# Kernel tuning notes

Hardware: AMD Instinct MI355X
Metric: run time of the kernel (lower is better)

Reference implementation:

```python
import jax, jax.numpy as jnp
import numpy as np
import math

C = 256          # embed_dims
NH = 8           # num_heads
FFN = 512        # int(embed_dims * ffn_ratio)
SPLITS = ((1, 1, 1), (2, 2, 2), (4, 4, 4), (8, 8, 8))
S = len(SPLITS)
B, Z, Hd, W = 1, 16, 16, 16


def setup_inputs() -> dict:
    key = jax.random.key(0)
    ks = jax.random.split(key, 10)
    n = lambda k, sh: jax.random.normal(k, sh, dtype=jnp.float32) * 0.02
    return {
        "x": jax.random.normal(ks[0], (B, C, Z, Hd, W), dtype=jnp.float32),
        "intra_wqkv": n(ks[1], (S, 3 * C, C)), "intra_bqkv": jnp.zeros((S, 3 * C), jnp.float32),
        "intra_wout": n(ks[2], (S, C, C)), "intra_bout": jnp.zeros((S, C), jnp.float32),
        "intra_ln_g": jnp.ones((S, C), jnp.float32), "intra_ln_b": jnp.zeros((S, C), jnp.float32),
        "inter_wqkv": n(ks[3], (S, 3 * C, C)), "inter_bqkv": jnp.zeros((S, 3 * C), jnp.float32),
        "inter_wout": n(ks[4], (S, C, C)), "inter_bout": jnp.zeros((S, C), jnp.float32),
        "inter_ln_g": jnp.ones((S, C), jnp.float32), "inter_ln_b": jnp.zeros((S, C), jnp.float32),
        "ffn_w1": n(ks[5], (S, FFN, C)), "ffn_b1": jnp.zeros((S, FFN), jnp.float32),
        "ffn_w2": n(ks[6], (S, C, FFN)), "ffn_b2": jnp.zeros((S, C), jnp.float32),
        "fuse_w": n(ks[7], (C, S * C)),
        "bn_g": jnp.ones((C,), jnp.float32), "bn_b": jnp.zeros((C,), jnp.float32),
    }


def _ln(x, g, b, eps=1e-5):
    m = x.mean(-1, keepdims=True)
    v = jnp.var(x, axis=-1, keepdims=True)
    return (x - m) / jnp.sqrt(v + eps) * g + b


def _mha(x, wqkv, bqkv, wout, bout):
    # x: [Bn, L, C]; torch nn.MultiheadAttention math (dropout=0)
    Bn, L, Cc = x.shape
    D = Cc // NH
    qkv = x @ wqkv.T + bqkv
    q, k, v = jnp.split(qkv, 3, axis=-1)
    q = q.reshape(Bn, L, NH, D)
    k = k.reshape(Bn, L, NH, D)
    v = v.reshape(Bn, L, NH, D)
    att = jax.nn.softmax(jnp.einsum('blhd,bmhd->bhlm', q, k) / math.sqrt(D), axis=-1)
    o = jnp.einsum('bhlm,bmhd->blhd', att, v).reshape(Bn, L, Cc)
    return o @ wout.T + bout


def reference(x, intra_wqkv, intra_bqkv, intra_wout, intra_bout, intra_ln_g, intra_ln_b,
              inter_wqkv, inter_bqkv, inter_wout, inter_bout, inter_ln_g, inter_ln_b,
              ffn_w1, ffn_b1, ffn_w2, ffn_b2, fuse_w, bn_g, bn_b):
    b, c, z, h, w = x.shape
    outs = []
    for i, (sx, sy, sz) in enumerate(SPLITS):
        bx, by, bz = w // sx, h // sy, z // sz  # dims divisible -> no padding path
        nb, bs = sx * sy * sz, bx * by * bz
        # carve blocks: [b,c,z,h,w] -> [b*nb, bs, c]
        xp = jnp.transpose(x, (0, 2, 3, 4, 1))
        t = xp.reshape(b, sz, bz, sy, by, sx, bx, c)
        t = jnp.transpose(t, (0, 1, 3, 5, 2, 4, 6, 7)).reshape(b * nb, bs, c)
        # intra-block self-attention + residual + LN
        t = _ln(t + _mha(t, intra_wqkv[i], intra_bqkv[i], intra_wout[i], intra_bout[i]),
                intra_ln_g[i], intra_ln_b[i])
        # inter-block attention on block means
        r = t.reshape(b, nb, bs, c).mean(2)  # [b, nb, c]
        r = _ln(r + _mha(r, inter_wqkv[i], inter_bqkv[i], inter_wout[i], inter_bout[i]),
                inter_ln_g[i], inter_ln_b[i])
        t = t.reshape(b, nb, bs, c) + r[:, :, None, :]
        # FFN (exact GELU) with residual
        hid = jax.nn.gelu(t @ ffn_w1[i].T + ffn_b1[i], approximate=False)
        t = t + (hid @ ffn_w2[i].T + ffn_b2[i])
        # un-carve back to [b,c,z,h,w]
        xo = t.reshape(b, sz, sy, sx, bz, by, bx, c)
        xo = jnp.transpose(xo, (0, 1, 4, 2, 5, 3, 6, 7)).reshape(b, z, h, w, c)
        xo = jnp.transpose(xo, (0, 4, 1, 2, 3))
        outs.append(xo + x)
    fused = jnp.concatenate(outs, axis=1)  # [b, 4c, z, h, w]
    y = jnp.einsum('bkzhw,ck->bczhw', fused, fuse_w)  # 1x1x1 Conv3d, no bias
    # BatchNorm3d in training mode: biased batch stats
    m = y.mean(axis=(0, 2, 3, 4))
    v = jnp.var(y, axis=(0, 2, 3, 4))
    bc = lambda a: a[None, :, None, None, None]
    y = (y - bc(m)) / jnp.sqrt(bc(v) + 1e-5) * bc(bn_g) + bc(bn_b)
    return jax.nn.relu(y)
```

## Files before the change

### kernel.cpp

```cpp
#include <hip/hip_runtime.h>
#include <math.h>

typedef __attribute__((ext_vector_type(8))) short s16x8;
typedef __attribute__((ext_vector_type(4))) short s16x4;
typedef __attribute__((ext_vector_type(4))) float f32x4;

__device__ __forceinline__ float b2f(unsigned short u) {
    union { unsigned u; float f; } x;
    x.u = ((unsigned)u) << 16;
    return x.f;
}
__device__ __forceinline__ unsigned short f2b(float f) {
    union { float f; unsigned u; } x;
    x.f = f;
    unsigned u = x.u;
    return (unsigned short)((u + 0x7FFFu + ((u >> 16) & 1u)) >> 16);
}
__device__ __forceinline__ f32x4 mfma16(s16x8 a, s16x8 b, f32x4 c) {
    return __builtin_amdgcn_mfma_f32_16x16x32_bf16(a, b, c, 0, 0, 0);
}
__device__ __forceinline__ float gelu_exact(float x) {
    return 0.5f * x * (1.0f + erff(x * 0.70710678118654752440f));
}
__device__ __forceinline__ void gload_lds16(const void* g, void* l) {
    __builtin_amdgcn_global_load_lds(
        (const __attribute__((address_space(1))) unsigned int*)g,
        (__attribute__((address_space(3))) unsigned int*)l, 16, 0, 0);
}
__device__ __forceinline__ int voxof(int blk, int pos, int logs, int lbsz) {
    int bm = (1 << lbsz) - 1, sm = (1 << logs) - 1;
    int ix = pos & bm, iy = (pos >> lbsz) & bm, iz = pos >> (2 * lbsz);
    int gx = blk & sm, gy = (blk >> logs) & sm, gz = blk >> (2 * logs);
    return (((gz << lbsz) + iz) << 8) + (((gy << lbsz) + iy) << 4) + ((gx << lbsz) + ix);
}
__device__ __forceinline__ int blkof(int v, int logs, int lbsz) {
    int gx = (v & 15) >> lbsz, gy = ((v >> 4) & 15) >> lbsz, gz = ((v >> 8) & 15) >> lbsz;
    return (((gz << logs) + gy) << logs) + gx;
}

__global__ __launch_bounds__(256) void prologue_k(
    const float* w0, const float* w1, const float* w2, const float* w3,
    const float* w4, const float* w5, const float* w6,
    unsigned short* __restrict__ wdst, const float* __restrict__ x,
    float* __restrict__ Xt, unsigned short* __restrict__ Xtb,
    float* __restrict__ Rb) {
    __shared__ float tile[32][33];
    int bx = blockIdx.x;
    if (bx < 3328) {
        int i = (bx * 256 + threadIdx.x) * 4;
        const float* s; int off;
        if (i < 786432)        { s = w0; off = 0; }
        else if (i < 1048576)  { s = w1; off = 786432; }
        else if (i < 1835008)  { s = w2; off = 1048576; }
        else if (i < 2097152)  { s = w3; off = 1835008; }
        else if (i < 2621440)  { s = w4; off = 2097152; }
        else if (i < 3145728)  { s = w5; off = 2621440; }
        else                   { s = w6; off = 3145728; }
        float4 v = *reinterpret_cast<const float4*>(s + (i - off));
        wdst[i + 0] = f2b(v.x); wdst[i + 1] = f2b(v.y);
        wdst[i + 2] = f2b(v.z); wdst[i + 3] = f2b(v.w);
    } else if (bx < 4352) {
        int t = bx - 3328;
        int v0 = (t & 127) * 32, c0 = (t >> 7) * 32;
        int tx = threadIdx.x & 31, ty = threadIdx.x >> 5;
#pragma unroll
        for (int j = 0; j < 32; j += 8)
            tile[ty + j][tx] = x[(size_t)(c0 + ty + j) * 4096 + v0 + tx];
        __syncthreads();
#pragma unroll
        for (int j = 0; j < 32; j += 8) {
            float v = tile[tx][ty + j];
            size_t o = (size_t)(v0 + ty + j) * 256 + c0 + tx;
            Xt[o] = v;
            Xtb[o] = f2b(v);
        }
    } else {
        int idx = ((bx - 4352) * 256 + threadIdx.x) * 4;
        if (idx < 149760) {
            float4 z4 = make_float4(0.f, 0.f, 0.f, 0.f);
            *reinterpret_cast<float4*>(Rb + idx) = z4;
        }
    }
}

template <int MFR, int HASB, int ACT, int OBF, int VT, int AF32, int EPI, int ZS>
__global__ __launch_bounds__(256) void gemm_k(
    const void* __restrict__ Aptr, const unsigned short* __restrict__ W,
    const float* __restrict__ bias, void* __restrict__ outp,
    int M, int N, int K, int ldC,
    long zsA, long zsW, long zsB, long zsC,
    unsigned short* __restrict__ vt, int mtot, long zsV,
    const void* __restrict__ Tresv, const float* __restrict__ RLNres,
    const float* __restrict__ Xres) {
    constexpr int BM = 32 * MFR;
    __shared__ unsigned short As[BM * 64];
    __shared__ unsigned short Ws[64 * 64];
    const int z = blockIdx.z;
    const int logs = (ZS == 1) ? z : 0;
    const int lbsz = (ZS == 1) ? (4 - z) : 4;
    const int goffc[4] = {0, 1, 9, 73};
    const int Mzc[4] = {1, 8, 64, 512};
    const int Me = (ZS == 2) ? Mzc[z] : M;
    const int m0 = blockIdx.y * BM, n0 = blockIdx.x * 64;
    if (ZS == 2 && m0 >= Me) return;
    const unsigned short* Ab = (const unsigned short*)Aptr +
        ((AF32 == 0 || AF32 == 3) ? ((size_t)z * zsA + (ZS == 2 ? (size_t)goffc[z] * K : 0)) : 0);
    const float* Af = (const float*)Aptr +
        ((AF32 == 1 || AF32 == 2) ? ((size_t)z * zsA + (ZS == 2 ? (size_t)goffc[z] * K : 0)) : 0);
    W += (size_t)z * zsW;
    const float* biasz = bias + (HASB ? (size_t)z * zsB : 0);
    char* outc = (char*)outp +
        ((size_t)z * zsC + (ZS == 2 ? (size_t)goffc[z] * ldC : 0)) * ((OBF || EPI) ? 2 : 4);
    const float* RLNz = RLNres + (ZS == 1 ? goffc[z] * 256 : 0);
    const unsigned short* Tzb = (const unsigned short*)Tresv + (ZS == 1 ? (size_t)z * 1048576 : 0);

    const int tid = threadIdx.x;
    const int wave = tid >> 6, lane = tid & 63;
    const int l15 = lane & 15, l4 = lane >> 4;
    const int wr = wave >> 1, wc = wave & 1;
    const int srow = lane >> 3;
    const int schunk = (lane & 7) ^ srow;
    f32x4 acc[MFR][2] = {};
    for (int k0 = 0; k0 < K; k0 += 64) {
        s16x8 sreg[MFR];
        if (AF32) {
#pragma unroll
            for (int i = 0; i < MFR; ++i) {
                int ca = wave * MFR + i;
                int gr = m0 + ca * 8 + srow;
                gr = gr < Me ? gr : (Me - 1);
                s16x8 pk;
                if (AF32 == 3) {
                    s16x8 tb = *reinterpret_cast<const s16x8*>(Ab + (size_t)gr * K + k0 + schunk * 8);
                    const float* rl = RLNz + (size_t)blkof(gr, logs, lbsz) * 256 + k0 + schunk * 8;
#pragma unroll
                    for (int e = 0; e < 8; ++e) pk[e] = (short)f2b(b2f((unsigned short)tb[e]) + rl[e]);
                } else {
                    const float* src = Af + (size_t)gr * K + k0 + schunk * 8;
                    float4 u = *reinterpret_cast<const float4*>(src);
                    float4 w2 = *reinterpret_cast<const float4*>(src + 4);
                    if (AF32 == 2) {
                        const float* rl = RLNz + (size_t)blkof(gr, logs, lbsz) * 256 + k0 + schunk * 8;
                        float4 a = *reinterpret_cast<const float4*>(rl);
                        float4 b = *reinterpret_cast<const float4*>(rl + 4);
                        u.x += a.x; u.y += a.y; u.z += a.z; u.w += a.w;
                        w2.x += b.x; w2.y += b.y; w2.z += b.z; w2.w += b.w;
                    }
                    pk[0] = (short)f2b(u.x); pk[1] = (short)f2b(u.y);
                    pk[2] = (short)f2b(u.z); pk[3] = (short)f2b(u.w);
                    pk[4] = (short)f2b(w2.x); pk[5] = (short)f2b(w2.y);
                    pk[6] = (short)f2b(w2.z); pk[7] = (short)f2b(w2.w);
                }
                sreg[i] = pk;
            }
        }
        __syncthreads();
        if (AF32) {
#pragma unroll
            for (int i = 0; i < MFR; ++i) {
                int ca = wave * MFR + i;
                *reinterpret_cast<s16x8*>((char*)As + ca * 1024 + lane * 16) = sreg[i];
            }
        } else {
#pragma unroll
            for (int i = 0; i < MFR; ++i) {
                int ca = wave * MFR + i;
                int gr = m0 + ca * 8 + srow;
                gr = gr < Me ? gr : (Me - 1);
                gload_lds16(Ab + (size_t)gr * K + k0 + schunk * 8, (char*)As + ca * 1024);
            }
        }
#pragma unroll
        for (int i = 0; i < 2; ++i) {
            int cb = wave * 2 + i;
            int gr = n0 + cb * 8 + srow;
            gload_lds16(W + (size_t)gr * K + k0 + schunk * 8, (char*)Ws + cb * 1024);
        }
        asm volatile("s_waitcnt vmcnt(0)" ::: "memory");
        __syncthreads();
#pragma unroll
        for (int ks = 0; ks < 2; ++ks) {
            s16x8 af[MFR], bf[2];
#pragma unroll
            for (int mf = 0; mf < MFR; ++mf) {
                int row = wr * (MFR * 16) + mf * 16 + l15;
                int ch = (ks * 4 + l4) ^ (row & 7);
                af[mf] = *reinterpret_cast<const s16x8*>((char*)As + row * 128 + ch * 16);
            }
#pragma unroll
            for (int nf = 0; nf < 2; ++nf) {
                int row = wc * 32 + nf * 16 + l15;
                int ch = (ks * 4 + l4) ^ (row & 7);
                bf[nf] = *reinterpret_cast<const s16x8*>((char*)Ws + row * 128 + ch * 16);
            }
#pragma unroll
            for (int mf = 0; mf < MFR; ++mf)
#pragma unroll
                for (int nf = 0; nf < 2; ++nf)
                    acc[mf][nf] = mfma16(af[mf], bf[nf], acc[mf][nf]);
        }
    }
#pragma unroll
    for (int nf = 0; nf < 2; ++nf) {
        int n = n0 + wc * 32 + nf * 16 + l15;
        float bv = HASB ? biasz[n] : 0.0f;
#pragma unroll
        for (int mf = 0; mf < MFR; ++mf) {
            float vr[4];
#pragma unroll
            for (int r = 0; r < 4; ++r) {
                int m = m0 + wr * (MFR * 16) + mf * 16 + l4 * 4 + r;
                float v = acc[mf][nf][r] + bv;
                if (ACT == 1) v = gelu_exact(v);
                vr[r] = v;
                if (m < Me) {
                    size_t co = (size_t)m * ldC + n;
                    if (EPI == 1) {
                        v += b2f(Tzb[(size_t)m * 256 + n]) +
                             RLNz[(size_t)blkof(m, logs, lbsz) * 256 + n] +
                             Xres[(size_t)m * 256 + n];
                        ((unsigned short*)outc)[co] = f2b(v);
                    } else if (OBF) {
                        ((unsigned short*)outc)[co] = f2b(v);
                    } else {
                        ((float*)outc)[co] = v;
                    }
                }
            }
            if (VT) {
                if ((ZS != 2 || z == 3) && n >= 512) {
                    s16x4 pk;
#pragma unroll
                    for (int r = 0; r < 4; ++r) pk[r] = (short)f2b(vr[r]);
                    int mb = m0 + wr * (MFR * 16) + mf * 16 + l4 * 4;
                    *reinterpret_cast<s16x4*>(vt + (size_t)z * zsV + (size_t)(n - 512) * mtot + mb) = pk;
                }
            }
        }
    }
}

__global__ __launch_bounds__(256) void attn_mfma2_k(
    const unsigned short* __restrict__ QKV, const unsigned short* __restrict__ Vtg,
    unsigned short* __restrict__ Opart, float* __restrict__ ML,
    int L, int Mtok, float cscale, int logs, int lbsz) {
    const int blk = blockIdx.z >> 3, h = blockIdx.z & 7;
    const int KS = gridDim.y, ks = blockIdx.y;
    const int wave = threadIdx.x >> 6, lane = threadIdx.x & 63;
    const int l15 = lane & 15, l4 = lane >> 4;
    const int q0 = blockIdx.x * 64 + wave * 16;

    __shared__ unsigned short Kl[2048];
    __shared__ unsigned short Vl[2048];
    __shared__ unsigned short Pl[4096];
    char* Plw = (char*)Pl + wave * 2048;

    const int qvox = voxof(blk, q0 + l15, logs, lbsz);
    s16x8 qf = *reinterpret_cast<const s16x8*>(QKV + (size_t)qvox * 768 + h * 32 + l4 * 8);

    f32x4 o0 = {}, o1 = {};
    float lR = 0.f;

    const int krow = threadIdx.x >> 2, kch = threadIdx.x & 3;
    const int kcol = (kch ^ (krow & 3)) * 8;
    const int vd = threadIdx.x >> 3, vc = threadIdx.x & 7;
    const int vrun = (vc ^ (vd & 7)) * 8;

    const int nt = L / (64 * KS);
    const int kb0 = ks * (L / KS);
    const int vstep = voxof(blk, kb0 + 64, logs, lbsz) - voxof(blk, kb0, logs, lbsz);
    const unsigned short* ksrc =
        QKV + (size_t)voxof(blk, kb0 + krow, logs, lbsz) * 768 + 256 + h * 32 + kcol;
    const unsigned short* vsrc =
        Vtg + (size_t)(h * 32 + vd) * Mtok + voxof(blk, kb0 + vrun, logs, lbsz);
    const size_t kadv = (size_t)vstep * 768;
    char* kdst = (char*)Kl + wave * 1024;
    char* vdst = (char*)Vl + wave * 1024;

    for (int it = 0; it < nt; ++it) {
        __syncthreads();
        gload_lds16(ksrc, kdst);
        gload_lds16(vsrc, vdst);
        ksrc += kadv; vsrc += vstep;
        asm volatile("s_waitcnt vmcnt(0)" ::: "memory");
        __syncthreads();

        f32x4 st[4];
        const f32x4 zz = {0.f, 0.f, 0.f, 0.f};
#pragma unroll
        for (int t4 = 0; t4 < 4; ++t4) {
            s16x8 kf = *reinterpret_cast<const s16x8*>(
                (char*)Kl + (t4 * 16 + l15) * 64 + ((l4 ^ (l15 & 3)) << 4));
            st[t4] = mfma16(kf, qf, zz);
        }
        float rsum = 0.f;
#pragma unroll
        for (int t4 = 0; t4 < 4; ++t4) {
            float p0 = exp2f(st[t4][0] * cscale);
            float p1 = exp2f(st[t4][1] * cscale);
            float p2 = exp2f(st[t4][2] * cscale);
            float p3 = exp2f(st[t4][3] * cscale);
            rsum += (p0 + p1) + (p2 + p3);
            unsigned d0, d1;
            asm("v_cvt_pk_bf16_f32 %0, %1, %2" : "=v"(d0) : "v"(p0), "v"(p1));
            asm("v_cvt_pk_bf16_f32 %0, %1, %2" : "=v"(d1) : "v"(p2), "v"(p3));
            int kcw = t4 * 2 + (l4 >> 1);
            uint2 w; w.x = d0; w.y = d1;
            *reinterpret_cast<uint2*>(Plw + l15 * 128 + ((kcw ^ (l15 & 7)) * 16) + (l4 & 1) * 8) = w;
        }
        rsum += __shfl_xor(rsum, 16);
        rsum += __shfl_xor(rsum, 32);
        lR += rsum;
#pragma unroll
        for (int kstep = 0; kstep < 2; ++kstep) {
            int kcr = kstep * 4 + l4;
            s16x8 pf = *reinterpret_cast<const s16x8*>(Plw + l15 * 128 + ((kcr ^ (l15 & 7)) * 16));
            s16x8 vf0 = *reinterpret_cast<const s16x8*>((char*)Vl + l15 * 128 + ((kcr ^ (l15 & 7)) * 16));
            s16x8 vf1 = *reinterpret_cast<const s16x8*>((char*)Vl + (16 + l15) * 128 + ((kcr ^ (l15 & 7)) * 16));
            o0 = mfma16(pf, vf0, o0);
            o1 = mfma16(pf, vf1, o1);
        }
    }
    float li[4];
#pragma unroll
    for (int r = 0; r < 4; ++r) li[r] = 1.0f / __shfl(lR, l4 * 4 + r);
#pragma unroll
    for (int r = 0; r < 4; ++r) {
        size_t row = ((size_t)ks * Mtok + voxof(blk, q0 + l4 * 4 + r, logs, lbsz)) * 256 + h * 32;
        Opart[row + l15] = f2b(o0[r] * li[r]);
        Opart[row + 16 + l15] = f2b(o1[r] * li[r]);
    }
    if (l4 == 0) ML[((size_t)ks * Mtok + qvox) * 8 + h] = lR;
}

__global__ __launch_bounds__(256) void attn_combine_k(
    const unsigned short* __restrict__ Opart, const float* __restrict__ ML,
    unsigned short* __restrict__ O, int TotTok, int KS,
    long zOp, long zML, long zO) {
    int z = blockIdx.y, row = blockIdx.x, c = threadIdx.x, h = c >> 5;
    Opart += (size_t)z * zOp;
    ML += (size_t)z * zML;
    O += (size_t)z * zO;
    float osum = 0.f, lsum = 0.f;
    for (int ks = 0; ks < KS; ++ks) {
        float l = ML[((size_t)ks * TotTok + row) * 8 + h];
        lsum += l;
        osum += l * b2f(Opart[((size_t)ks * TotTok + row) * 256 + c]);
    }
    O[(size_t)row * 256 + c] = f2b(osum / lsum);
}

__global__ __launch_bounds__(256) void attn_f32i_k(const unsigned short* __restrict__ QKVA2,
                                                   unsigned short* __restrict__ ObfA,
                                                   float scale) {
    int y = blockIdx.y;
    int z, blk, h, L, logs, lbsz;
    if (y < 512) { z = 2; blk = y >> 3; h = y & 7; L = 64; logs = 2; lbsz = 2; }
    else {
        z = 3; int yy = y - 512; blk = yy >> 3; h = yy & 7; L = 8; logs = 3; lbsz = 1;
        if (blockIdx.x != 0) return;
    }
    const unsigned short* QKV = QKVA2 + (size_t)(z - 2) * 3145728;
    unsigned short* O = ObfA + (size_t)z * 1048576;
    const int tid = threadIdx.x, r = tid >> 3, li = tid & 7;
    const int qr = blockIdx.x * 32 + r;
    const int qrc = (qr < L) ? qr : 0;
    const int qvox = voxof(blk, qrc, logs, lbsz);

    float q[32];
    {
        const unsigned short* qp = QKV + (size_t)qvox * 768 + h * 32;
#pragma unroll
        for (int d8 = 0; d8 < 4; ++d8) {
            s16x8 v = *reinterpret_cast<const s16x8*>(qp + d8 * 8);
#pragma unroll
            for (int e = 0; e < 8; ++e) q[d8 * 8 + e] = b2f((unsigned short)v[e]) * scale;
        }
    }
    float l = 0.f;
    float o[32];
#pragma unroll
    for (int d = 0; d < 32; ++d) o[d] = 0.f;

    __shared__ float Kl[32][36];
    __shared__ float Vl[32][36];
    const int krow = tid >> 3, kd = (tid & 7) * 4;
    const int nt = (L + 31) / 32;
    for (int kt = 0; kt < nt; ++kt) {
        int key = kt * 32 + krow;
        float4 kv = make_float4(0.f, 0.f, 0.f, 0.f);
        float4 vv = make_float4(0.f, 0.f, 0.f, 0.f);
        if (key < L) {
            int kvox = voxof(blk, key, logs, lbsz);
            s16x4 k4 = *reinterpret_cast<const s16x4*>(QKV + (size_t)kvox * 768 + 256 + h * 32 + kd);
            s16x4 v4 = *reinterpret_cast<const s16x4*>(QKV + (size_t)kvox * 768 + 512 + h * 32 + kd);
            kv = make_float4(b2f((unsigned short)k4[0]), b2f((unsigned short)k4[1]),
                             b2f((unsigned short)k4[2]), b2f((unsigned short)k4[3]));
            vv = make_float4(b2f((unsigned short)v4[0]), b2f((unsigned short)v4[1]),
                             b2f((unsigned short)v4[2]), b2f((unsigned short)v4[3]));
        }
        __syncthreads();
        Kl[krow][kd + 0] = kv.x; Kl[krow][kd + 1] = kv.y;
        Kl[krow][kd + 2] = kv.z; Kl[krow][kd + 3] = kv.w;
        Vl[krow][kd + 0] = vv.x; Vl[krow][kd + 1] = vv.y;
        Vl[krow][kd + 2] = vv.z; Vl[krow][kd + 3] = vv.w;
        __syncthreads();
#pragma unroll
        for (int j = 0; j < 4; ++j) {
            int kk = j * 8 + li;
            float acc = 0.f;
#pragma unroll
            for (int d4 = 0; d4 < 8; ++d4) {
                float4 k4 = *reinterpret_cast<const float4*>(&Kl[kk][d4 * 4]);
                acc += q[d4 * 4 + 0] * k4.x + q[d4 * 4 + 1] * k4.y +
                       q[d4 * 4 + 2] * k4.z + q[d4 * 4 + 3] * k4.w;
            }
            float p = (kt * 32 + kk < L) ? __expf(acc) : 0.f;
            l += p;
#pragma unroll
            for (int d4 = 0; d4 < 8; ++d4) {
                float4 v4 = *reinterpret_cast<const float4*>(&Vl[kk][d4 * 4]);
                o[d4 * 4 + 0] += p * v4.x; o[d4 * 4 + 1] += p * v4.y;
                o[d4 * 4 + 2] += p * v4.z; o[d4 * 4 + 3] += p * v4.w;
            }
        }
    }
#pragma unroll
    for (int d = 0; d < 32; ++d) {
        o[d] += __shfl_xor(o[d], 1);
        o[d] += __shfl_xor(o[d], 2);
        o[d] += __shfl_xor(o[d], 4);
    }
    l += __shfl_xor(l, 1);
    l += __shfl_xor(l, 2);
    l += __shfl_xor(l, 4);
    if (qr < L) {
        float inv = 1.0f / l;
        size_t orow = (size_t)qvox * 256 + h * 32;
#pragma unroll
        for (int qd = 0; qd < 4; ++qd) O[orow + li * 4 + qd] = f2b(o[li * 4 + qd] * inv);
    }
}

__global__ __launch_bounds__(256) void attn_f32b_k(const unsigned short* __restrict__ RQKV,
                                                   unsigned short* __restrict__ RO,
                                                   float scale) {
    const int y = blockIdx.y;
    const int z = y >> 3, h = y & 7;
    const int Lz[3] = {1, 8, 64};
    const int goffc[3] = {0, 1, 9};
    const int L = Lz[z];
    const unsigned short* base = RQKV + (size_t)goffc[z] * 768;
    unsigned short* O = RO + (size_t)goffc[z] * 256;
    const int tid = threadIdx.x;
    const int r = tid >> 3, li = tid & 7;
    const int qr = blockIdx.x * 32 + r;
    const int qrc = (qr < L) ? qr : 0;

    float q[32];
    {
        const unsigned short* qp = base + (size_t)qrc * 768 + h * 32;
#pragma unroll
        for (int d8 = 0; d8 < 4; ++d8) {
            s16x8 v = *reinterpret_cast<const s16x8*>(qp + d8 * 8);
#pragma unroll
            for (int e = 0; e < 8; ++e) q[d8 * 8 + e] = b2f((unsigned short)v[e]) * scale;
        }
    }
    float l = 0.f;
    float o[32];
#pragma unroll
    for (int d = 0; d < 32; ++d) o[d] = 0.f;

    __shared__ float Kl[32][36];
    __shared__ float Vl[32][36];
    const int krow = tid >> 3, kd = (tid & 7) * 4;
    const int nt = (L + 31) / 32;
    for (int kt = 0; kt < nt; ++kt) {
        int key = kt * 32 + krow;
        float4 kv = make_float4(0.f, 0.f, 0.f, 0.f);
        float4 vv = make_float4(0.f, 0.f, 0.f, 0.f);
        if (key < L) {
            s16x4 k4 = *reinterpret_cast<const s16x4*>(base + (size_t)key * 768 + 256 + h * 32 + kd);
            s16x4 v4 = *reinterpret_cast<const s16x4*>(base + (size_t)key * 768 + 512 + h * 32 + kd);
            kv = make_float4(b2f((unsigned short)k4[0]), b2f((unsigned short)k4[1]),
                             b2f((unsigned short)k4[2]), b2f((unsigned short)k4[3]));
            vv = make_float4(b2f((unsigned short)v4[0]), b2f((unsigned short)v4[1]),
                             b2f((unsigned short)v4[2]), b2f((unsigned short)v4[3]));
        }
        __syncthreads();
        Kl[krow][kd + 0] = kv.x; Kl[krow][kd + 1] = kv.y;
        Kl[krow][kd + 2] = kv.z; Kl[krow][kd + 3] = kv.w;
        Vl[krow][kd + 0] = vv.x; Vl[krow][kd + 1] = vv.y;
        Vl[krow][kd + 2] = vv.z; Vl[krow][kd + 3] = vv.w;
        __syncthreads();
#pragma unroll
        for (int j = 0; j < 4; ++j) {
            int kk = j * 8 + li;
            float acc = 0.f;
#pragma unroll
            for (int d4 = 0; d4 < 8; ++d4) {
                float4 k4 = *reinterpret_cast<const float4*>(&Kl[kk][d4 * 4]);
                acc += q[d4 * 4 + 0] * k4.x + q[d4 * 4 + 1] * k4.y +
                       q[d4 * 4 + 2] * k4.z + q[d4 * 4 + 3] * k4.w;
            }
            float p = (kt * 32 + kk < L) ? __expf(acc) : 0.f;
            l += p;
#pragma unroll
            for (int d4 = 0; d4 < 8; ++d4) {
                float4 v4 = *reinterpret_cast<const float4*>(&Vl[kk][d4 * 4]);
                o[d4 * 4 + 0] += p * v4.x; o[d4 * 4 + 1] += p * v4.y;
                o[d4 * 4 + 2] += p * v4.z; o[d4 * 4 + 3] += p * v4.w;
            }
        }
    }
#pragma unroll
    for (int d = 0; d < 32; ++d) {
        o[d] += __shfl_xor(o[d], 1);
        o[d] += __shfl_xor(o[d], 2);
        o[d] += __shfl_xor(o[d], 4);
    }
    l += __shfl_xor(l, 1);
    l += __shfl_xor(l, 2);
    l += __shfl_xor(l, 4);
    if (qr < L) {
        float inv = 1.0f / l;
        size_t orow = (size_t)qr * 256 + h * 32;
#pragma unroll
        for (int qd = 0; qd < 4; ++qd) O[orow + li * 4 + qd] = f2b(o[li * 4 + qd] * inv);
    }
}

__global__ __launch_bounds__(256) void add_ln_b_k(const float* __restrict__ X,
                                                  const unsigned short* __restrict__ T1b,
                                                  const float* __restrict__ g,
                                                  const float* __restrict__ b,
                                                  unsigned short* __restrict__ Tb) {
    int row = blockIdx.x & 4095, z = blockIdx.x >> 12, t = threadIdx.x;
    float v = X[row * 256 + t] + b2f(T1b[(size_t)z * 1048576 + row * 256 + t]);
    float s1 = v, s2 = v * v;
#pragma unroll
    for (int mask = 1; mask < 64; mask <<= 1) {
        s1 += __shfl_xor(s1, mask);
        s2 += __shfl_xor(s2, mask);
    }
    __shared__ float w1[4], w2[4];
    int wv = t >> 6, ln = t & 63;
    if (ln == 0) { w1[wv] = s1; w2[wv] = s2; }
    __syncthreads();
    float tot1 = w1[0] + w1[1] + w1[2] + w1[3];
    float tot2 = w2[0] + w2[1] + w2[2] + w2[3];
    float mean = tot1 * (1.0f / 256.0f);
    float var = tot2 * (1.0f / 256.0f) - mean * mean;
    float rstd = rsqrtf(var + 1e-5f);
    Tb[(size_t)z * 1048576 + row * 256 + t] =
        f2b((v - mean) * rstd * g[z * 256 + t] + b[z * 256 + t]);
}

__global__ __launch_bounds__(256) void add_ln_i_k(const float* __restrict__ Rb_all,
                                                  const float* __restrict__ R1_all,
                                                  const float* __restrict__ g,
                                                  const float* __restrict__ b,
                                                  float* __restrict__ RLN_all) {
    int row = blockIdx.x, t = threadIdx.x;
    int z = (row == 0) ? 0 : (row < 9 ? 1 : (row < 73 ? 2 : 3));
    float v = Rb_all[row * 256 + t] + R1_all[row * 256 + t];
    float s1 = v, s2 = v * v;
#pragma unroll
    for (int mask = 1; mask < 64; mask <<= 1) {
        s1 += __shfl_xor(s1, mask);
        s2 += __shfl_xor(s2, mask);
    }
    __shared__ float w1[4], w2[4];
    int wv = t >> 6, ln = t & 63;
    if (ln == 0) { w1[wv] = s1; w2[wv] = s2; }
    __syncthreads();
    float tot1 = w1[0] + w1[1] + w1[2] + w1[3];
    float tot2 = w2[0] + w2[1] + w2[2] + w2[3];
    float mean = tot1 * (1.0f / 256.0f);
    float var = tot2 * (1.0f / 256.0f) - mean * mean;
    float rstd = rsqrtf(var + 1e-5f);
    RLN_all[row * 256 + t] = (v - mean) * rstd * g[z * 256 + t] + b[z * 256 + t];
}

__global__ __launch_bounds__(256) void block_mean_b_k(const unsigned short* __restrict__ Tb_all,
                                                      float* __restrict__ Rb_all) {
    int bx = blockIdx.x, c = threadIdx.x;
    int z, blk, ch, rpc;
    float inv_bs;
    if (bx < 128)      { z = 0; blk = 0;               ch = bx;              rpc = 32; inv_bs = 1.0f / 4096.0f; }
    else if (bx < 256) { int l = bx - 128; z = 1; blk = l >> 4; ch = l & 15; rpc = 32; inv_bs = 1.0f / 512.0f; }
    else if (bx < 384) { int l = bx - 256; z = 2; blk = l >> 1; ch = l & 1;  rpc = 32; inv_bs = 1.0f / 64.0f; }
    else               { int l = bx - 384; z = 3; blk = l;      ch = 0;      rpc = 8;  inv_bs = 1.0f / 8.0f; }
    const int goffc[4] = {0, 1, 9, 73};
    const int logs = z, lbsz = 4 - z;
    const unsigned short* T = Tb_all + (size_t)z * 1048576;
    float* R = Rb_all + (size_t)(goffc[z] + blk) * 256;
    int p0 = ch * rpc;
    float sum = 0.f;
    for (int p = p0; p < p0 + rpc; ++p)
        sum += b2f(T[(size_t)voxof(blk, p, logs, lbsz) * 256 + c]);
    atomicAdd(&R[c], sum * inv_bs);
}

__global__ __launch_bounds__(256) void bn_stats_k(const float* __restrict__ Yt,
                                                  float* __restrict__ MV) {
    int b0 = blockIdx.x * 16, c = threadIdx.x;
    float s1 = 0.f, s2 = 0.f;
#pragma unroll
    for (int j = 0; j < 16; ++j) {
        float v = Yt[(size_t)(b0 + j) * 256 + c];
        s1 += v; s2 += v * v;
    }
    atomicAdd(&MV[c], s1);
    atomicAdd(&MV[256 + c], s2);
}

__global__ __launch_bounds__(256) void bn_apply_k(const float* __restrict__ Yt,
                                                  const float* __restrict__ MV,
                                                  const float* __restrict__ g,
                                                  const float* __restrict__ b,
                                                  float* __restrict__ outp) {
    int c = blockIdx.x, t = threadIdx.x;
    float mean = MV[c] * (1.0f / 4096.0f);
    float var = MV[256 + c] * (1.0f / 4096.0f) - mean * mean;
    float rstd = rsqrtf(var + 1e-5f);
    float gg = g[c] * rstd, bb = b[c] - mean * gg;
    for (int it = 0; it < 16; ++it) {
        int v = it * 256 + t;
        float y = Yt[(size_t)v * 256 + c];
        float rr = y * gg + bb;
        outp[(size_t)c * 4096 + v] = rr > 0.f ? rr : 0.f;
    }
}

extern "C" void kernel_launch(void* const* d_in, const int* in_sizes, int n_in,
                              void* d_out, int out_size, void* d_ws, size_t ws_size,
                              hipStream_t stream) {
    (void)in_sizes; (void)n_in; (void)out_size; (void)ws_size;
    const float* x          = (const float*)d_in[0];
    const float* intra_bqkv = (const float*)d_in[2];
    const float* intra_bout = (const float*)d_in[4];
    const float* intra_ln_g = (const float*)d_in[5];
    const float* intra_ln_b = (const float*)d_in[6];
    const float* inter_bqkv = (const float*)d_in[8];
    const float* inter_bout = (const float*)d_in[10];
    const float* inter_ln_g = (const float*)d_in[11];
    const float* inter_ln_b = (const float*)d_in[12];
    const float* ffn_b1     = (const float*)d_in[14];
    const float* ffn_b2     = (const float*)d_in[16];
    const float* bn_g       = (const float*)d_in[18];
    const float* bn_b       = (const float*)d_in[19];
    float* out = (float*)d_out;

    float* ws = (float*)d_ws;
    unsigned short* OUTt  = (unsigned short*)ws;
    float* Xt             = ws + 2097152;
    unsigned short* Xtb   = (unsigned short*)(ws + 3145728);
    unsigned short* QKVA2 = (unsigned short*)(ws + 3670016);
    unsigned short* ObfA  = (unsigned short*)(ws + 6815744);
    unsigned short* T1A   = (unsigned short*)(ws + 8912896);
    unsigned short* TAb   = (unsigned short*)(ws + 11010048);
    float* Rb_all         = ws + 13107200;
    unsigned short* RQKVa = (unsigned short*)(ws + 13256960);
    unsigned short* RObA  = (unsigned short*)(ws + 13481600);
    float* R1A            = ws + 13556480;
    float* RLN_all        = ws + 13706240;
    unsigned short* WB    = (unsigned short*)(ws + 13856000);
    unsigned short* VtgA  = (unsigned short*)(ws + 15559936);
    unsigned short* Vtgr  = (unsigned short*)(ws + 16608512);
    float* MLbuf          = ws + 16674048;
    unsigned short* OpartI = T1A;
    unsigned short* OpartR = T1A;
    unsigned short* HidA   = QKVA2;
    float* MV              = MLbuf;
    float* Yt              = Xt;

    unsigned short* WBq  = WB;
    unsigned short* WBo  = WB + 786432;
    unsigned short* WBiq = WB + 1048576;
    unsigned short* WBio = WB + 1835008;
    unsigned short* WBf1 = WB + 2097152;
    unsigned short* WBf2 = WB + 2621440;
    unsigned short* WBfu = WB + 3145728;

    const float scale = 0.17677669529663687f;
    const float cscale = scale * 1.44269504088896f;
    const long ZC = 1048576;

    prologue_k<<<4499, 256, 0, stream>>>((const float*)d_in[1], (const float*)d_in[3],
                                         (const float*)d_in[7], (const float*)d_in[9],
                                         (const float*)d_in[13], (const float*)d_in[15],
                                         (const float*)d_in[17], WB, x, Xt, Xtb, Rb_all);

    gemm_k<4, 1, 0, 1, 1, 0, 0, 0><<<dim3(12, 32, 2), 256, 0, stream>>>(
        Xtb, WBq, intra_bqkv, QKVA2, 4096, 768, 256, 768,
        0, 196608, 768, 3145728, VtgA, 4096, 1048576, TAb, Rb_all, Xt);
    attn_mfma2_k<<<dim3(64, 4, 8), 256, 0, stream>>>(
        QKVA2, VtgA, OpartI, MLbuf, 4096, 4096, cscale, 0, 4);
    attn_mfma2_k<<<dim3(8, 4, 64), 256, 0, stream>>>(
        QKVA2 + 3145728, VtgA + 1048576, OpartI + 4194304, MLbuf + 131072,
        512, 4096, cscale, 1, 3);
    attn_combine_k<<<dim3(4096, 2), 256, 0, stream>>>(
        OpartI, MLbuf, ObfA, 4096, 4, 4194304, 131072, 1048576);
    gemm_k<4, 1, 0, 1, 0, 0, 0, 0><<<dim3(12, 32, 2), 256, 0, stream>>>(
        Xtb, WBq + 2 * 196608, intra_bqkv + 2 * 768, QKVA2, 4096, 768, 256, 768,
        0, 196608, 768, 3145728, nullptr, 0, 0, TAb, Rb_all, Xt);
    attn_f32i_k<<<dim3(2, 4608), 256, 0, stream>>>(QKVA2, ObfA, scale);
    gemm_k<2, 1, 0, 1, 0, 0, 0, 0><<<dim3(4, 64, 4), 256, 0, stream>>>(
        ObfA, WBo, intra_bout, T1A, 4096, 256, 256, 256,
        ZC, 65536, 256, ZC, nullptr, 0, 0, TAb, Rb_all, Xt);
    add_ln_b_k<<<16384, 256, 0, stream>>>(Xt, T1A, intra_ln_g, intra_ln_b, TAb);
    block_mean_b_k<<<896, 256, 0, stream>>>(TAb, Rb_all);
    gemm_k<2, 1, 0, 1, 1, 1, 0, 2><<<dim3(12, 8, 4), 256, 0, stream>>>(
        Rb_all, WBiq, inter_bqkv, RQKVa, 512, 768, 256, 768,
        0, 196608, 768, 0, Vtgr, 512, 0, TAb, Rb_all, Xt);
    attn_mfma2_k<<<dim3(8, 8, 8), 256, 0, stream>>>(
        RQKVa + (size_t)73 * 768, Vtgr, OpartR, MLbuf, 512, 512, cscale, 0, 4);
    attn_f32b_k<<<dim3(2, 24), 256, 0, stream>>>(RQKVa, RObA, scale);
    attn_combine_k<<<dim3(512, 1), 256, 0, stream>>>(
        OpartR, MLbuf, RObA + (size_t)73 * 256, 512, 8, 0, 0, 0);
    gemm_k<2, 1, 0, 0, 0, 0, 0, 2><<<dim3(4, 8, 4), 256, 0, stream>>>(
        RObA, WBio, inter_bout, R1A, 512, 256, 256, 256,
        0, 65536, 256, 0, nullptr, 0, 0, TAb, Rb_all, Xt);
    add_ln_i_k<<<585, 256, 0, stream>>>(Rb_all, R1A, inter_ln_g, inter_ln_b, RLN_all);
    gemm_k<4, 1, 1, 1, 0, 3, 0, 1><<<dim3(8, 32, 4), 256, 0, stream>>>(
        TAb, WBf1, ffn_b1, HidA, 4096, 512, 256, 512,
        ZC, 131072, 512, 2097152, nullptr, 0, 0, TAb, RLN_all, Xt);
    gemm_k<2, 1, 0, 1, 0, 0, 1, 1><<<dim3(4, 64, 4), 256, 0, stream>>>(
        HidA, WBf2, ffn_b2, OUTt, 4096, 256, 512, 1024,
        2097152, 131072, 256, 256, nullptr, 0, 0, TAb, RLN_all, Xt);
    gemm_k<2, 0, 0, 0, 0, 0, 0, 0><<<dim3(4, 64, 1), 256, 0, stream>>>(
        OUTt, WBfu, nullptr, Yt, 4096, 256, 1024, 256,
        0, 0, 0, 0, nullptr, 0, 0, TAb, Rb_all, Xt);
    hipMemsetAsync(MV, 0, 512 * sizeof(float), stream);
    bn_stats_k<<<256, 256, 0, stream>>>(Yt, MV);
    bn_apply_k<<<256, 256, 0, stream>>>(Yt, MV, bn_g, bn_b, out);
}
```

Baseline: 310.9 us.

## Fuse split-0/1 attention launches and route split-2 attention through MFMA path

Merges the two MFMA attention launches for the first two splits into one flat-grid kernel. The split-2 attention (block length 64) moves from a scalar fp32 kernel onto the MFMA attention core, with a variant that gathers V with two 4-element loads. For that, the second QKV GEMM now also writes the transposed V, and split 3 gets its own small fp32 kernel. The aim is fewer launches and tensor-core use for split 2, at the cost of extra V-transpose writes and unaligned V gathers.

```diff
diff --git a/kernel.cpp b/kernel.cpp
--- a/kernel.cpp
+++ b/kernel.cpp
@@ -240,19 +240,15 @@
     }
 }
 
-__global__ __launch_bounds__(256) void attn_mfma2_k(
-    const unsigned short* __restrict__ QKV, const unsigned short* __restrict__ Vtg,
-    unsigned short* __restrict__ Opart, float* __restrict__ ML,
-    int L, int Mtok, float cscale, int logs, int lbsz) {
-    const int blk = blockIdx.z >> 3, h = blockIdx.z & 7;
-    const int KS = gridDim.y, ks = blockIdx.y;
+template <int VST>
+__device__ __forceinline__ void attn_core(
+    const unsigned short* QKV, const unsigned short* Vtg,
+    unsigned short* Opart, float* ML,
+    int L, int Mtok, float cscale, int logs, int lbsz,
+    int blk, int h, int KS, int ks, int q0,
+    unsigned short* Kl, unsigned short* Vl, unsigned short* Pl) {
     const int wave = threadIdx.x >> 6, lane = threadIdx.x & 63;
     const int l15 = lane & 15, l4 = lane >> 4;
-    const int q0 = blockIdx.x * 64 + wave * 16;
-
-    __shared__ unsigned short Kl[2048];
-    __shared__ unsigned short Vl[2048];
-    __shared__ unsigned short Pl[4096];
     char* Plw = (char*)Pl + wave * 2048;
 
     const int qvox = voxof(blk, q0 + l15, logs, lbsz);
@@ -268,11 +264,14 @@
 
     const int nt = L / (64 * KS);
     const int kb0 = ks * (L / KS);
-    const int vstep = voxof(blk, kb0 + 64, logs, lbsz) - voxof(blk, kb0, logs, lbsz);
+    const int vstep = (nt > 1)
+        ? (voxof(blk, kb0 + 64, logs, lbsz) - voxof(blk, kb0, logs, lbsz)) : 0;
     const unsigned short* ksrc =
         QKV + (size_t)voxof(blk, kb0 + krow, logs, lbsz) * 768 + 256 + h * 32 + kcol;
     const unsigned short* vsrc =
         Vtg + (size_t)(h * 32 + vd) * Mtok + voxof(blk, kb0 + vrun, logs, lbsz);
+    const unsigned short* vsrc2 =
+        Vtg + (size_t)(h * 32 + vd) * Mtok + voxof(blk, kb0 + vrun + 4, logs, lbsz);
     const size_t kadv = (size_t)vstep * 768;
     char* kdst = (char*)Kl + wave * 1024;
     char* vdst = (char*)Vl + wave * 1024;
@@ -280,8 +279,17 @@
     for (int it = 0; it < nt; ++it) {
         __syncthreads();
         gload_lds16(ksrc, kdst);
-        gload_lds16(vsrc, vdst);
-        ksrc += kadv; vsrc += vstep;
+        if (VST == 0) {
+            gload_lds16(vsrc, vdst);
+        } else {
+            s16x4 lo = *reinterpret_cast<const s16x4*>(vsrc);
+            s16x4 hi = *reinterpret_cast<const s16x4*>(vsrc2);
+            s16x8 vv;
+            vv[0] = lo[0]; vv[1] = lo[1]; vv[2] = lo[2]; vv[3] = lo[3];
+            vv[4] = hi[0]; vv[5] = hi[1]; vv[6] = hi[2]; vv[7] = hi[3];
+            *reinterpret_cast<s16x8*>((char*)Vl + threadIdx.x * 16) = vv;
+        }
+        ksrc += kadv; vsrc += vstep; vsrc2 += vstep;
         asm volatile("s_waitcnt vmcnt(0)" ::: "memory");
         __syncthreads();
 
@@ -331,6 +339,45 @@
         Opart[row + 16 + l15] = f2b(o1[r] * li[r]);
     }
     if (l4 == 0) ML[((size_t)ks * Mtok + qvox) * 8 + h] = lR;
+}
+
+__global__ __launch_bounds__(256) void attn_fused01_k(
+    const unsigned short* __restrict__ QKVA2, const unsigned short* __restrict__ VtgA,
+    unsigned short* __restrict__ OpartI, float* __restrict__ MLbuf, float cscale) {
+    __shared__ unsigned short Kl[2048];
+    __shared__ unsigned short Vl[2048];
+    __shared__ unsigned short Pl[4096];
+    int bid = blockIdx.x;
+    int plane, xb, ks, zz, L, logs, lbsz;
+    if (bid < 2048) {
+        plane = 0; xb = bid & 63; ks = (bid >> 6) & 3; zz = bid >> 8;
+        L = 4096; logs = 0; lbsz = 4;
+    } else {
+        int b2 = bid - 2048;
+        plane = 1; xb = b2 & 7; ks = (b2 >> 3) & 3; zz = b2 >> 5;
+        L = 512; logs = 1; lbsz = 3;
+    }
+    const int blk = zz >> 3, h = zz & 7;
+    const int wave = threadIdx.x >> 6;
+    const int q0 = xb * 64 + wave * 16;
+    attn_core<0>(QKVA2 + (size_t)plane * 3145728, VtgA + (size_t)plane * 1048576,
+                 OpartI + (size_t)plane * 4194304, MLbuf + (size_t)plane * 131072,
+                 L, 4096, cscale, logs, lbsz, blk, h, 4, ks, q0, Kl, Vl, Pl);
+}
+
+template <int VST>
+__global__ __launch_bounds__(256) void attn_mfma2_k(
+    const unsigned short* __restrict__ QKV, const unsigned short* __restrict__ Vtg,
+    unsigned short* __restrict__ Opart, float* __restrict__ ML,
+    int L, int Mtok, float cscale, int logs, int lbsz) {
+    __shared__ unsigned short Kl[2048];
+    __shared__ unsigned short Vl[2048];
+    __shared__ unsigned short Pl[4096];
+    const int blk = blockIdx.z >> 3, h = blockIdx.z & 7;
+    const int wave = threadIdx.x >> 6;
+    const int q0 = blockIdx.x * 64 + wave * 16;
+    attn_core<VST>(QKV, Vtg, Opart, ML, L, Mtok, cscale, logs, lbsz,
+                   blk, h, gridDim.y, blockIdx.y, q0, Kl, Vl, Pl);
 }
 
 __global__ __launch_bounds__(256) void attn_combine_k(
@@ -350,20 +397,14 @@
     O[(size_t)row * 256 + c] = f2b(osum / lsum);
 }
 
-__global__ __launch_bounds__(256) void attn_f32i_k(const unsigned short* __restrict__ QKVA2,
-                                                   unsigned short* __restrict__ ObfA,
-                                                   float scale) {
-    int y = blockIdx.y;
-    int z, blk, h, L, logs, lbsz;
-    if (y < 512) { z = 2; blk = y >> 3; h = y & 7; L = 64; logs = 2; lbsz = 2; }
-    else {
-        z = 3; int yy = y - 512; blk = yy >> 3; h = yy & 7; L = 8; logs = 3; lbsz = 1;
-        if (blockIdx.x != 0) return;
-    }
-    const unsigned short* QKV = QKVA2 + (size_t)(z - 2) * 3145728;
-    unsigned short* O = ObfA + (size_t)z * 1048576;
+__global__ __launch_bounds__(256) void attn_f32z3_k(const unsigned short* __restrict__ QKV,
+                                                    unsigned short* __restrict__ O,
+                                                    float scale) {
+    const int y = blockIdx.y;
+    const int blk = y >> 3, h = y & 7;
+    const int L = 8, logs = 3, lbsz = 1;
     const int tid = threadIdx.x, r = tid >> 3, li = tid & 7;
-    const int qr = blockIdx.x * 32 + r;
+    const int qr = r;
     const int qrc = (qr < L) ? qr : 0;
     const int qvox = voxof(blk, qrc, logs, lbsz);
 
@@ -385,44 +426,40 @@
     __shared__ float Kl[32][36];
     __shared__ float Vl[32][36];
     const int krow = tid >> 3, kd = (tid & 7) * 4;
-    const int nt = (L + 31) / 32;
-    for (int kt = 0; kt < nt; ++kt) {
-        int key = kt * 32 + krow;
-        float4 kv = make_float4(0.f, 0.f, 0.f, 0.f);
-        float4 vv = make_float4(0.f, 0.f, 0.f, 0.f);
-        if (key < L) {
-            int kvox = voxof(blk, key, logs, lbsz);
-            s16x4 k4 = *reinterpret_cast<const s16x4*>(QKV + (size_t)kvox * 768 + 256 + h * 32 + kd);
-            s16x4 v4 = *reinterpret_cast<const s16x4*>(QKV + (size_t)kvox * 768 + 512 + h * 32 + kd);
-            kv = make_float4(b2f((unsigned short)k4[0]), b2f((unsigned short)k4[1]),
-                             b2f((unsigned short)k4[2]), b2f((unsigned short)k4[3]));
-            vv = make_float4(b2f((unsigned short)v4[0]), b2f((unsigned short)v4[1]),
-                             b2f((unsigned short)v4[2]), b2f((unsigned short)v4[3]));
-        }
-        __syncthreads();
-        Kl[krow][kd + 0] = kv.x; Kl[krow][kd + 1] = kv.y;
-        Kl[krow][kd + 2] = kv.z; Kl[krow][kd + 3] = kv.w;
-        Vl[krow][kd + 0] = vv.x; Vl[krow][kd + 1] = vv.y;
-        Vl[krow][kd + 2] = vv.z; Vl[krow][kd + 3] = vv.w;
-        __syncthreads();
-#pragma unroll
-        for (int j = 0; j < 4; ++j) {
-            int kk = j * 8 + li;
-            float acc = 0.f;
-#pragma unroll
-            for (int d4 = 0; d4 < 8; ++d4) {
-                float4 k4 = *reinterpret_cast<const float4*>(&Kl[kk][d4 * 4]);
-                acc += q[d4 * 4 + 0] * k4.x + q[d4 * 4 + 1] * k4.y +
-                       q[d4 * 4 + 2] * k4.z + q[d4 * 4 + 3] * k4.w;
-            }
-            float p = (kt * 32 + kk < L) ? __expf(acc) : 0.f;
-            l += p;
-#pragma unroll
-            for (int d4 = 0; d4 < 8; ++d4) {
-                float4 v4 = *reinterpret_cast<const float4*>(&Vl[kk][d4 * 4]);
-                o[d4 * 4 + 0] += p * v4.x; o[d4 * 4 + 1] += p * v4.y;
-                o[d4 * 4 + 2] += p * v4.z; o[d4 * 4 + 3] += p * v4.w;
-            }
+    float4 kv = make_float4(0.f, 0.f, 0.f, 0.f);
+    float4 vv = make_float4(0.f, 0.f, 0.f, 0.f);
+    if (krow < L) {
+        int kvox = voxof(blk, krow, logs, lbsz);
+        s16x4 k4 = *reinterpret_cast<const s16x4*>(QKV + (size_t)kvox * 768 + 256 + h * 32 + kd);
+        s16x4 v4 = *reinterpret_cast<const s16x4*>(QKV + (size_t)kvox * 768 + 512 + h * 32 + kd);
+        kv = make_float4(b2f((unsigned short)k4[0]), b2f((unsigned short)k4[1]),
+                         b2f((unsigned short)k4[2]), b2f((unsigned short)k4[3]));
+        vv = make_float4(b2f((unsigned short)v4[0]), b2f((unsigned short)v4[1]),
+                         b2f((unsigned short)v4[2]), b2f((unsigned short)v4[3]));
+    }
+    __syncthreads();
+    Kl[krow][kd + 0] = kv.x; Kl[krow][kd + 1] = kv.y;
+    Kl[krow][kd + 2] = kv.z; Kl[krow][kd + 3] = kv.w;
+    Vl[krow][kd + 0] = vv.x; Vl[krow][kd + 1] = vv.y;
+    Vl[krow][kd + 2] = vv.z; Vl[krow][kd + 3] = vv.w;
+    __syncthreads();
+#pragma unroll
+    for (int j = 0; j < 4; ++j) {
+        int kk = j * 8 + li;
+        float acc = 0.f;
+#pragma unroll
+        for (int d4 = 0; d4 < 8; ++d4) {
+            float4 k4 = *reinterpret_cast<const float4*>(&Kl[kk][d4 * 4]);
+            acc += q[d4 * 4 + 0] * k4.x + q[d4 * 4 + 1] * k4.y +
+                   q[d4 * 4 + 2] * k4.z + q[d4 * 4 + 3] * k4.w;
+        }
+        float p = (kk < L) ? __expf(acc) : 0.f;
+        l += p;
+#pragma unroll
+        for (int d4 = 0; d4 < 8; ++d4) {
+            float4 v4 = *reinterpret_cast<const float4*>(&Vl[kk][d4 * 4]);
+            o[d4 * 4 + 0] += p * v4.x; o[d4 * 4 + 1] += p * v4.y;
+            o[d4 * 4 + 2] += p * v4.z; o[d4 * 4 + 3] += p * v4.w;
         }
     }
 #pragma unroll
@@ -696,17 +733,15 @@
     gemm_k<4, 1, 0, 1, 1, 0, 0, 0><<<dim3(12, 32, 2), 256, 0, stream>>>(
         Xtb, WBq, intra_bqkv, QKVA2, 4096, 768, 256, 768,
         0, 196608, 768, 3145728, VtgA, 4096, 1048576, TAb, Rb_all, Xt);
-    attn_mfma2_k<<<dim3(64, 4, 8), 256, 0, stream>>>(
-        QKVA2, VtgA, OpartI, MLbuf, 4096, 4096, cscale, 0, 4);
-    attn_mfma2_k<<<dim3(8, 4, 64), 256, 0, stream>>>(
-        QKVA2 + 3145728, VtgA + 1048576, OpartI + 4194304, MLbuf + 131072,
-        512, 4096, cscale, 1, 3);
+    attn_fused01_k<<<4096, 256, 0, stream>>>(QKVA2, VtgA, OpartI, MLbuf, cscale);
     attn_combine_k<<<dim3(4096, 2), 256, 0, stream>>>(
         OpartI, MLbuf, ObfA, 4096, 4, 4194304, 131072, 1048576);
-    gemm_k<4, 1, 0, 1, 0, 0, 0, 0><<<dim3(12, 32, 2), 256, 0, stream>>>(
+    gemm_k<4, 1, 0, 1, 1, 0, 0, 0><<<dim3(12, 32, 2), 256, 0, stream>>>(
         Xtb, WBq + 2 * 196608, intra_bqkv + 2 * 768, QKVA2, 4096, 768, 256, 768,
-        0, 196608, 768, 3145728, nullptr, 0, 0, TAb, Rb_all, Xt);
-    attn_f32i_k<<<dim3(2, 4608), 256, 0, stream>>>(QKVA2, ObfA, scale);
+        0, 196608, 768, 3145728, VtgA, 4096, 1048576, TAb, Rb_all, Xt);
+    attn_mfma2_k<1><<<dim3(1, 1, 512), 256, 0, stream>>>(
+        QKVA2, VtgA, ObfA + 2 * ZC, MLbuf, 64, 4096, cscale, 2, 2);
+    attn_f32z3_k<<<dim3(1, 4096), 256, 0, stream>>>(QKVA2 + 3145728, ObfA + 3 * ZC, scale);
     gemm_k<2, 1, 0, 1, 0, 0, 0, 0><<<dim3(4, 64, 4), 256, 0, stream>>>(
         ObfA, WBo, intra_bout, T1A, 4096, 256, 256, 256,
         ZC, 65536, 256, ZC, nullptr, 0, 0, TAb, Rb_all, Xt);
@@ -715,7 +750,7 @@
     gemm_k<2, 1, 0, 1, 1, 1, 0, 2><<<dim3(12, 8, 4), 256, 0, stream>>>(
         Rb_all, WBiq, inter_bqkv, RQKVa, 512, 768, 256, 768,
         0, 196608, 768, 0, Vtgr, 512, 0, TAb, Rb_all, Xt);
-    attn_mfma2_k<<<dim3(8, 8, 8), 256, 0, stream>>>(
+    attn_mfma2_k<0><<<dim3(8, 8, 8), 256, 0, stream>>>(
         RQKVa + (size_t)73 * 768, Vtgr, OpartR, MLbuf, 512, 512, cscale, 0, 4);
     attn_f32b_k<<<dim3(2, 24), 256, 0, stream>>>(RQKVa, RObA, scale);
     attn_combine_k<<<dim3(512, 1), 256, 0, stream>>>(
```

Measured after the change: 264.1 us. 1.18x faster.
